# Performance work log

Measured on AMD Instinct MI355X. Metric: run time of the kernel, lower is better.

Reference implementation:

```python
import math
import jax, jax.numpy as jnp
import numpy as np

NEG = -1.0e10  # matches LARGE_NUMBER padding in the original
K_SUBSET = 8
N_SAMPLES = 2


def log_conv(aL, aR, K):
    """Log-space convolution of two count distributions, truncated to counts 0..K-1.
    aL, aR: [..., K] log-values; returns c[m] = logsumexp_j aL[j] + aR[m-j]."""
    jj = jnp.arange(K)[:, None]
    mm = jnp.arange(K)[None, :]
    idx = mm - jj  # [K(j), K(m)]
    valid = idx >= 0
    aRg = aR[..., jnp.clip(idx, 0, K - 1)]  # [..., K, K]
    t = aL[..., :, None] + jnp.where(valid, aRg, NEG)
    return jax.nn.logsumexp(t, axis=-2)


def up_pass(theta, k):
    """theta: [B, N] logits (N power of two). Returns list of per-level log-ESP
    tables, levels[l]: [B, N/2^l, k+1]; levels[-1][:,0,j] = log e_j(exp theta)."""
    B, N = theta.shape
    K = k + 1
    leaf = jnp.full((B, N, K), NEG, theta.dtype)
    leaf = leaf.at[..., 0].set(0.0).at[..., 1].set(theta)
    levels = [leaf]
    a = leaf
    while a.shape[1] > 1:
        a = log_conv(a[:, 0::2], a[:, 1::2], K)
        levels.append(a)
    return levels


def down_marginals(levels, theta, k):
    """Exact inclusion marginals P(x_i=1 | sum=k) via tree forward-backward."""
    K = k + 1
    B = theta.shape[0]
    ext = jnp.full((B, 1, K), NEG, theta.dtype).at[..., 0].set(0.0)
    for lvl in range(len(levels) - 2, -1, -1):
        a = levels[lvl]
        aL, aR = a[:, 0::2], a[:, 1::2]
        extL = log_conv(ext, aR, K)  # ESP of everything outside left subtree
        extR = log_conv(ext, aL, K)
        ext = jnp.stack([extL, extR], axis=2).reshape(B, a.shape[1], K)
    logZ = levels[-1][:, 0, k]  # log e_k over all items
    # P(x_i=1) = exp(theta_i) * e_{k-1}(others) / e_k(all)
    return jnp.exp(theta + ext[..., k - 1] - logZ[:, None])


def sample_counts(levels, k, n_samples, key):
    """Top-down exact sampling of k-subsets; returns leaf counts [S, B, N] in {0,1}."""
    K = k + 1
    B = levels[0].shape[0]
    counts = jnp.full((n_samples, B, 1), k, jnp.int32)
    jj = jnp.arange(K)
    for lvl in range(len(levels) - 2, -1, -1):
        a = levels[lvl]
        aL, aR = a[:, 0::2], a[:, 1::2]
        n = aL.shape[1]
        idx = counts[..., None] - jj  # desired right-count, [S,B,n,K]
        valid = idx >= 0
        aRg = jnp.take_along_axis(
            jnp.broadcast_to(aR[None], (n_samples, B, n, K)),
            jnp.clip(idx, 0, k), axis=-1)
        logits = aL[None] + jnp.where(valid, aRg, NEG)
        key, sub = jax.random.split(key)
        g = jax.random.gumbel(sub, logits.shape, logits.dtype)
        cL = jnp.argmax(logits + g, axis=-1).astype(jnp.int32)
        cR = counts - cL
        counts = jnp.stack([cL, cR], axis=-1).reshape(n_samples, B, 2 * n)
    return counts


def setup_inputs() -> dict:
    key = jax.random.key(0)
    scores = jax.random.normal(key, (8192, 32, 8), dtype=jnp.float32)
    return {"scores": scores}


def reference(scores):
    nnodes, choices, ensemble = scores.shape
    k = min(K_SUBSET, choices)
    flat = jnp.transpose(scores, (0, 2, 1)).reshape(nnodes * ensemble, choices)
    N = 2 ** math.ceil(math.log2(choices))
    if N > choices:
        flat = jnp.concatenate(
            [flat, jnp.full((flat.shape[0], N - choices), NEG, flat.dtype)], axis=1)
    levels = up_pass(flat, k)
    marg_flat = down_marginals(levels, flat, k)[:, :choices]  # [B, choices]
    marginals = jnp.transpose(
        marg_flat.reshape(nnodes, ensemble, choices), (0, 2, 1))  # [nnodes, choices, ensemble]
    counts = sample_counts(levels, k, N_SAMPLES, jax.random.key(42))
    counts = counts[:, :, :choices].astype(scores.dtype)
    samples = jnp.transpose(
        counts.reshape(N_SAMPLES, nnodes, ensemble, choices), (0, 1, 3, 2))
    # straight-through: hard samples forward, marginal gradients backward
    samples = jax.lax.stop_gradient(samples - marginals[None]) + marginals[None]
    return samples, marginals
```

## Files before the change

### kernel.cpp

```cpp
#include <hip/hip_runtime.h>
#include <stdint.h>


__host__ __device__ __forceinline__ void tf2x32(uint32_t k0, uint32_t k1,
                                                uint32_t x0, uint32_t x1,
                                                uint32_t& y0, uint32_t& y1) {
  const uint32_t ks[3] = {k0, k1, k0 ^ k1 ^ 0x1BD11BDAu};
  x0 += ks[0]; x1 += ks[1];
  const int R0[4] = {13, 15, 26, 6};
  const int R1[4] = {17, 29, 16, 24};
#pragma unroll
  for (int i = 0; i < 5; ++i) {
    const int* R = (i & 1) ? R1 : R0;
#pragma unroll
    for (int rr = 0; rr < 4; ++rr) {
      x0 += x1;
      x1 = (x1 << R[rr]) | (x1 >> (32 - R[rr]));
      x1 ^= x0;
    }
    x0 += ks[(i + 1) % 3];
    x1 += ks[(i + 2) % 3] + (uint32_t)(i + 1);
  }
  y0 = x0; y1 = x1;
}

struct TFKeys { uint32_t v[10]; };

__device__ __forceinline__ float gumbel_draw(uint32_t sk0, uint32_t sk1,
                                             uint32_t f) {
  uint32_t y0, y1;
  tf2x32(sk0, sk1, 0u, f, y0, y1);
  uint32_t bits = y0 ^ y1;
  uint32_t fb = (bits >> 9) | 0x3f800000u;
  float u = __uint_as_float(fb) - 1.0f;
  const float tiny = 1.17549435e-38f;
  float rr = fmaxf(tiny, u + tiny);
  return -logf(-logf(rr));
}

template<bool FAST> __device__ __forceinline__ float expT(float x) {
  return FAST ? __expf(x) : expf(x);
}
template<bool FAST> __device__ __forceinline__ float logT(float x) {
  return FAST ? __logf(x) : logf(x);
}

template<int SIN, int SOUT, bool FAST, bool LS>
__device__ __forceinline__ void conv_level(const float (&aL)[SIN],
                                           const float (&aR)[SIN],
                                           float (&o)[SOUT]) {
#pragma unroll
  for (int m = 1; m < SOUT; ++m) {
    if (LS && m == SOUT - 1) { o[m] = aL[SIN - 1] + aR[SIN - 1]; continue; }
    const int jlo = (m - (SIN - 1) > 0) ? (m - (SIN - 1)) : 0;
    const int jhi = (m < SIN - 1) ? m : (SIN - 1);
    float t[SIN];
#pragma unroll
    for (int j = 0; j < SIN; ++j)
      if (j >= jlo && j <= jhi) t[j] = aL[j] + aR[m - j];
    float amax = t[jlo];
#pragma unroll
    for (int j = 0; j < SIN; ++j)
      if (j > jlo && j <= jhi) amax = fmaxf(amax, t[j]);
    float s = 0.0f;
#pragma unroll
    for (int j = 0; j < SIN; ++j)
      if (j >= jlo && j <= jhi) s += expT<FAST>(t[j] - amax);
    o[m] = logT<FAST>(s) + amax;
  }
}

template<int SSIB, int MLO, int MHI, bool FAST>
__device__ __forceinline__ void ext_level(const float (&ein)[8],
                                          const float* sib, float (&eo)[8]) {
#pragma unroll
  for (int m = MLO; m <= MHI; ++m) {
    const int jlo = (m - (SSIB - 1) > 0) ? (m - (SSIB - 1)) : 0;
    float t[8];
#pragma unroll
    for (int j = 0; j < 8; ++j)
      if (j >= jlo && j <= m) t[j] = ein[j] + sib[m - j];
    float amax = t[jlo];
#pragma unroll
    for (int j = 0; j < 8; ++j)
      if (j > jlo && j <= m) amax = fmaxf(amax, t[j]);
    float s = 0.0f;
#pragma unroll
    for (int j = 0; j < 8; ++j)
      if (j >= jlo && j <= m) s += expT<FAST>(t[j] - amax);
    eo[m] = logT<FAST>(s) + amax;
  }
}

#define ENT 128

__global__ __launch_bounds__(64, 2) void simple_sampler_kernel(
    const float* __restrict__ scores, float* __restrict__ out,
    int nnodes, TFKeys keys) {
  const int lane = threadIdx.x;
  const int p = lane & 1;
  const int r = lane >> 1;
  const int row = blockIdx.x * 32 + r;
  const int node = row >> 3, e = row & 7;
  const int B = nnodes * 8;

  __shared__ float tab[ENT * 32];
#define L(E) tab[(E) * 32 + r]

  float th[16];
  const float* sc = scores + node * 256 + e + p * 128;
#pragma unroll
  for (int c = 0; c < 16; ++c) th[c] = sc[c * 8];
#pragma unroll
  for (int c = 0; c < 16; ++c) L(16 * p + c) = th[c];

  float l1r[8], th2r[8];
#pragma unroll
  for (int n1l = 0; n1l < 8; ++n1l) {
    float tL = th[2 * n1l], tR = th[2 * n1l + 1];
    float amax = fmaxf(tR, tL);
    float s = expf(tR - amax) + expf(tL - amax);
    l1r[n1l] = logf(s) + amax;
    th2r[n1l] = tL + tR;
    int n1 = 8 * p + n1l;
    L(32 + n1) = l1r[n1l];
    L(48 + n1) = th2r[n1l];
  }
  float l2r[4][5];
#pragma unroll
  for (int n2l = 0; n2l < 4; ++n2l) {
    float aL[3] = {0.0f, l1r[2 * n2l], th2r[2 * n2l]};
    float aR[3] = {0.0f, l1r[2 * n2l + 1], th2r[2 * n2l + 1]};
    float o5[5];
    conv_level<3, 5, false, true>(aL, aR, o5);
    l2r[n2l][0] = 0.0f;
    int n2 = 4 * p + n2l;
#pragma unroll
    for (int m = 1; m < 5; ++m) { l2r[n2l][m] = o5[m]; L(64 + n2 * 4 + m - 1) = o5[m]; }
  }
  float l3r[2][9];
#pragma unroll
  for (int n3l = 0; n3l < 2; ++n3l) {
    float o9[9];
    conv_level<5, 9, false, true>(l2r[2 * n3l], l2r[2 * n3l + 1], o9);
    l3r[n3l][0] = 0.0f;
    int n3 = 2 * p + n3l;
#pragma unroll
    for (int m = 1; m < 9; ++m) { l3r[n3l][m] = o9[m]; L(96 + n3 * 8 + m - 1) = o9[m]; }
  }

  __builtin_amdgcn_wave_barrier();

  float A0[9], A1[9];
  {
    float l4o[9];
    conv_level<9, 9, false, false>(l3r[0], l3r[1], l4o);
    A0[0] = 0.0f; A1[0] = 0.0f;
#pragma unroll
    for (int m = 1; m < 9; ++m) {
      float own = l4o[m];
      float oth = __shfl_xor(own, 1);
      A0[m] = p ? oth : own;
      A1[m] = p ? own : oth;
    }
  }

  float logZ;
  {
    float tv[9];
#pragma unroll
    for (int j = 0; j < 9; ++j) tv[j] = A0[j] + A1[8 - j];
    float amax = tv[0];
#pragma unroll
    for (int j = 1; j < 9; ++j) amax = fmaxf(amax, tv[j]);
    float s = 0.0f;
#pragma unroll
    for (int j = 0; j < 9; ++j) s += __expf(tv[j] - amax);
    logZ = __logf(s) + amax;
  }

  {
    float e4v[8];
    e4v[0] = 0.0f;
#pragma unroll
    for (int m = 1; m < 8; ++m) e4v[m] = p ? A0[m] : A1[m];
    float* mb = out + 2 * B * 32 + node * 256 + e;
#pragma unroll
    for (int n3l = 0; n3l < 2; ++n3l) {
      float e3[8];
      ext_level<9, 0, 7, true>(e4v, l3r[n3l ^ 1], e3);
#pragma unroll
      for (int c2 = 0; c2 < 2; ++c2) {
        const int n2l = 2 * n3l + c2;
        float e2v[8];
        ext_level<5, 4, 7, true>(e3, l2r[n2l ^ 1], e2v);
#pragma unroll
        for (int c1i = 0; c1i < 2; ++c1i) {
          const int n1l = 2 * n2l + c1i;
          float sib1[3] = {0.0f, l1r[n1l ^ 1], th2r[n1l ^ 1]};
          float e1m[8];
          ext_level<3, 6, 7, true>(e2v, sib1, e1m);
          const int colL = 16 * p + 2 * n1l;
          {
            float t6 = e1m[6] + th[2 * n1l + 1];
            float t7 = e1m[7];
            float amax = fmaxf(t6, t7);
            float s = __expf(t6 - amax) + __expf(t7 - amax);
            mb[colL * 8] = __expf((th[2 * n1l] + (__logf(s) + amax)) - logZ);
          }
          {
            float t6 = e1m[6] + th[2 * n1l];
            float t7 = e1m[7];
            float amax = fmaxf(t6, t7);
            float s = __expf(t6 - amax) + __expf(t7 - amax);
            mb[(colL + 1) * 8] = __expf((th[2 * n1l + 1] + (__logf(s) + amax)) - logZ);
          }
        }
      }
    }
  }

  const uint32_t t9 = (uint32_t)(p * B + row) * 9u;
  int c0, c1;
  {
    float best = 0.0f; int bj = 0;
#pragma unroll
    for (int j = 0; j < 9; ++j) {
      float g = gumbel_draw(keys.v[0], keys.v[1], t9 + (uint32_t)j);
      float v = (A0[j] + A1[8 - j]) + g;
      if (j == 0) { best = v; } else if (v > best) { best = v; bj = j; }
    }
    c0 = bj; c1 = 8 - bj;
  }
  int c1v[4];
  {
    const int n0 = c0 ? c0 + 1 : 0;
    const int n1c = c1 ? c1 + 1 : 0;
    const int tot = n0 + n1c;
    float b0 = -3.0e38f, b1 = -3.0e38f;
    int j0 = 0, j1 = 0;
    for (int t = 0; t < tot; ++t) {
      const bool is1 = (t >= n0);
      const int j = is1 ? (t - n0) : t;
      const int c = is1 ? c1 : c0;
      const int i = is1 ? 1 : 0;
      const int idx = c - j;
      float a = (j == 0) ? 0.0f : L(96 + 16 * i + j - 1);
      float b = (idx == 0) ? 0.0f : L(96 + 16 * i + 8 + idx - 1);
      float g = gumbel_draw(keys.v[2], keys.v[3],
                            2u * t9 + (uint32_t)(9 * i + j));
      float v = (a + b) + g;
      if (is1) { if (v > b1) { b1 = v; j1 = j; } }
      else     { if (v > b0) { b0 = v; j0 = j; } }
    }
    c1v[0] = j0; c1v[1] = c0 - j0; c1v[2] = j1; c1v[3] = c1 - j1;
  }
  uint32_t pk2 = 0;
  {
#pragma unroll
    for (int i = 0; i < 4; ++i) {
      int c = c1v[i];
      float best = -3.0e38f; int bj2 = 0;
#pragma unroll
      for (int j = 0; j < 5; ++j) {
        float g = gumbel_draw(keys.v[4], keys.v[5],
                              4u * t9 + (uint32_t)(i * 9 + j));
        int idx = c - j;
        int cl = min(max(idx, 1), 4);
        float b = L(64 + (2 * i + 1) * 4 + cl - 1);
        float bf = (idx == 0) ? 0.0f : b;
        float a = (j == 0) ? 0.0f : L(64 + (2 * i) * 4 + j - 1);
        float v = (a + bf) + g;
        if (idx >= 0 && idx <= 4 && v > best) { best = v; bj2 = j; }
      }
      pk2 |= ((uint32_t)bj2 << (8 * i)) | ((uint32_t)(c - bj2) << (8 * i + 4));
    }
  }
  uint64_t pk64 = 0;
  {
    const uint32_t sk0 = keys.v[6], sk1 = keys.v[7];
    const uint32_t fb0 = 8u * t9;
#pragma unroll 2
    for (int i = 0; i < 8; ++i) {
      int c = (int)((pk2 >> (4 * i)) & 15u);
      float aL1 = L(32 + 2 * i), aL2 = L(48 + 2 * i);
      float bR1 = L(32 + 2 * i + 1), bR2 = L(48 + 2 * i + 1);
      uint32_t fb = fb0 + (uint32_t)(i * 9);
      float best = -3.0e38f; int bj3 = 0;
#pragma unroll
      for (int j = 0; j < 3; ++j) {
        float g = gumbel_draw(sk0, sk1, fb + (uint32_t)j);
        int idx = c - j;
        float bf = (idx == 1) ? bR1 : ((idx == 2) ? bR2 : 0.0f);
        float af = (j == 0) ? 0.0f : ((j == 1) ? aL1 : aL2);
        float v = (af + bf) + g;
        if (idx >= 0 && idx <= 2 && v > best) { best = v; bj3 = j; }
      }
      pk64 |= ((uint64_t)(uint32_t)bj3 << (8 * i)) |
              ((uint64_t)(uint32_t)(c - bj3) << (8 * i + 4));
    }
  }
  {
    const uint32_t sk0 = keys.v[8], sk1 = keys.v[9];
    const uint32_t fb0 = 16u * t9;
    float* bs = out + p * (B * 32) + node * 256 + e;
    uint64_t lst = 0; int m4 = 0;
#pragma unroll
    for (int i = 0; i < 16; ++i) {
      int c = (int)((uint32_t)(pk64 >> (4 * i)) & 15u);
      if (c == 1) {
        lst |= ((uint64_t)(uint32_t)i) << (4 * m4);
        ++m4;
      } else {
        int bj = c >> 1;
        bs[16 * i] = (float)bj;
        bs[16 * i + 8] = (float)(c - bj);
      }
    }
    for (int tt = 0; tt < m4; ++tt) {
      int i = (int)((lst >> (4 * tt)) & 15u);
      float thL = L(2 * i);
      float thR = L(2 * i + 1);
      uint32_t fb = fb0 + (uint32_t)(i * 9);
      float g0 = gumbel_draw(sk0, sk1, fb);
      float g1 = gumbel_draw(sk0, sk1, fb + 1u);
      int bj = ((thL + g1) > (thR + g0)) ? 1 : 0;
      bs[16 * i] = (float)bj;
      bs[16 * i + 8] = (float)(1 - bj);
    }
  }
#undef L
}

extern "C" void kernel_launch(void* const* d_in, const int* in_sizes, int n_in,
                              void* d_out, int out_size, void* d_ws, size_t ws_size,
                              hipStream_t stream) {
  const float* scores = (const float*)d_in[0];
  float* out = (float*)d_out;
  const int nnodes = in_sizes[0] / (32 * 8);
  const int B = nnodes * 8;

  TFKeys K;
  uint32_t k0 = 0u, k1 = 42u;
  for (int t = 0; t < 5; ++t) {
    uint32_t n0, n1, s0, s1;
    tf2x32(k0, k1, 0u, 0u, n0, n1);
    tf2x32(k0, k1, 0u, 1u, s0, s1);
    K.v[2 * t] = s0; K.v[2 * t + 1] = s1;
    k0 = n0; k1 = n1;
  }

  dim3 grid((unsigned)(B / 32)), block(64);
  hipLaunchKernelGGL(simple_sampler_kernel, grid, block, 0, stream,
                     scores, out, nnodes, K);
}
```

Before: 114.4 us.

## Split each row across four lanes instead of two and enlarge blocks

Each row (node, ensemble) is now handled by four lanes rather than two. Each lane holds 8 logits and does a quarter of the up-pass tree, exchanging level-3 tables with a shuffle. Sampling is split across lanes by sample index and by left/right half of the tree, with the root choice combined through a shuffle. Blocks grow from one wave to four waves with per-wave shared tables, which raises parallelism and cuts per-thread registers, at the cost of extra shuffles and some redundant root work.

Measured after the change: 115.2 us. About the same (+0.6%).

```diff
diff --git a/kernel.cpp b/kernel.cpp
--- a/kernel.cpp
+++ b/kernel.cpp
@@ -94,67 +94,81 @@
 
 #define ENT 128
 
-__global__ __launch_bounds__(64, 2) void simple_sampler_kernel(
+__global__ __launch_bounds__(256, 4) void simple_sampler_kernel(
     const float* __restrict__ scores, float* __restrict__ out,
     int nnodes, TFKeys keys) {
-  const int lane = threadIdx.x;
-  const int p = lane & 1;
-  const int r = lane >> 1;
-  const int row = blockIdx.x * 32 + r;
+  const int wl = threadIdx.x & 63;
+  const int w  = threadIdx.x >> 6;
+  const int q = wl & 3;
+  const int r = wl >> 2;
+  const int p = q & 1;
+  const int g = q >> 1;
+  const int row = blockIdx.x * 64 + w * 16 + r;
   const int node = row >> 3, e = row & 7;
   const int B = nnodes * 8;
 
-  __shared__ float tab[ENT * 32];
-#define L(E) tab[(E) * 32 + r]
-
-  float th[16];
-  const float* sc = scores + node * 256 + e + p * 128;
-#pragma unroll
-  for (int c = 0; c < 16; ++c) th[c] = sc[c * 8];
-#pragma unroll
-  for (int c = 0; c < 16; ++c) L(16 * p + c) = th[c];
-
-  float l1r[8], th2r[8];
-#pragma unroll
-  for (int n1l = 0; n1l < 8; ++n1l) {
+  __shared__ float tab[4 * ENT * 16];
+  float* tw = tab + w * (ENT * 16);
+#define L(E) tw[(E) * 16 + r]
+
+  float th[8];
+  const float* sc = scores + node * 256 + e + (16 * p + 8 * g) * 8;
+#pragma unroll
+  for (int c = 0; c < 8; ++c) th[c] = sc[c * 8];
+#pragma unroll
+  for (int c = 0; c < 8; ++c) L(16 * p + 8 * g + c) = th[c];
+
+  float l1r[4], th2r[4];
+#pragma unroll
+  for (int n1l = 0; n1l < 4; ++n1l) {
     float tL = th[2 * n1l], tR = th[2 * n1l + 1];
     float amax = fmaxf(tR, tL);
     float s = expf(tR - amax) + expf(tL - amax);
     l1r[n1l] = logf(s) + amax;
     th2r[n1l] = tL + tR;
-    int n1 = 8 * p + n1l;
+    int n1 = 8 * p + 4 * g + n1l;
     L(32 + n1) = l1r[n1l];
     L(48 + n1) = th2r[n1l];
   }
-  float l2r[4][5];
-#pragma unroll
-  for (int n2l = 0; n2l < 4; ++n2l) {
+  float l2r[2][5];
+#pragma unroll
+  for (int n2l = 0; n2l < 2; ++n2l) {
     float aL[3] = {0.0f, l1r[2 * n2l], th2r[2 * n2l]};
     float aR[3] = {0.0f, l1r[2 * n2l + 1], th2r[2 * n2l + 1]};
     float o5[5];
     conv_level<3, 5, false, true>(aL, aR, o5);
     l2r[n2l][0] = 0.0f;
-    int n2 = 4 * p + n2l;
+    int n2 = 4 * p + 2 * g + n2l;
 #pragma unroll
     for (int m = 1; m < 5; ++m) { l2r[n2l][m] = o5[m]; L(64 + n2 * 4 + m - 1) = o5[m]; }
   }
-  float l3r[2][9];
-#pragma unroll
-  for (int n3l = 0; n3l < 2; ++n3l) {
+  float l3r[9];
+  {
     float o9[9];
-    conv_level<5, 9, false, true>(l2r[2 * n3l], l2r[2 * n3l + 1], o9);
-    l3r[n3l][0] = 0.0f;
-    int n3 = 2 * p + n3l;
-#pragma unroll
-    for (int m = 1; m < 9; ++m) { l3r[n3l][m] = o9[m]; L(96 + n3 * 8 + m - 1) = o9[m]; }
+    conv_level<5, 9, false, true>(l2r[0], l2r[1], o9);
+    l3r[0] = 0.0f;
+    int n3 = 2 * p + g;
+#pragma unroll
+    for (int m = 1; m < 9; ++m) { l3r[m] = o9[m]; L(96 + n3 * 8 + m - 1) = o9[m]; }
   }
 
   __builtin_amdgcn_wave_barrier();
 
+  float l3s[9];
+  l3s[0] = 0.0f;
+#pragma unroll
+  for (int m = 1; m < 9; ++m) l3s[m] = __shfl_xor(l3r[m], 2);
+
   float A0[9], A1[9];
   {
+    float aLp[9], aRp[9];
+#pragma unroll
+    for (int m = 0; m < 9; ++m) {
+      aLp[m] = g ? l3s[m] : l3r[m];
+      aRp[m] = g ? l3r[m] : l3s[m];
+    }
     float l4o[9];
-    conv_level<9, 9, false, false>(l3r[0], l3r[1], l4o);
+    conv_level<9, 9, false, false>(aLp, aRp, l4o);
     A0[0] = 0.0f; A1[0] = 0.0f;
 #pragma unroll
     for (int m = 1; m < 9; ++m) {
@@ -185,140 +199,141 @@
 #pragma unroll
     for (int m = 1; m < 8; ++m) e4v[m] = p ? A0[m] : A1[m];
     float* mb = out + 2 * B * 32 + node * 256 + e;
-#pragma unroll
-    for (int n3l = 0; n3l < 2; ++n3l) {
-      float e3[8];
-      ext_level<9, 0, 7, true>(e4v, l3r[n3l ^ 1], e3);
-#pragma unroll
-      for (int c2 = 0; c2 < 2; ++c2) {
-        const int n2l = 2 * n3l + c2;
-        float e2v[8];
-        ext_level<5, 4, 7, true>(e3, l2r[n2l ^ 1], e2v);
-#pragma unroll
-        for (int c1i = 0; c1i < 2; ++c1i) {
-          const int n1l = 2 * n2l + c1i;
-          float sib1[3] = {0.0f, l1r[n1l ^ 1], th2r[n1l ^ 1]};
-          float e1m[8];
-          ext_level<3, 6, 7, true>(e2v, sib1, e1m);
-          const int colL = 16 * p + 2 * n1l;
-          {
-            float t6 = e1m[6] + th[2 * n1l + 1];
-            float t7 = e1m[7];
-            float amax = fmaxf(t6, t7);
-            float s = __expf(t6 - amax) + __expf(t7 - amax);
-            mb[colL * 8] = __expf((th[2 * n1l] + (__logf(s) + amax)) - logZ);
-          }
-          {
-            float t6 = e1m[6] + th[2 * n1l];
-            float t7 = e1m[7];
-            float amax = fmaxf(t6, t7);
-            float s = __expf(t6 - amax) + __expf(t7 - amax);
-            mb[(colL + 1) * 8] = __expf((th[2 * n1l + 1] + (__logf(s) + amax)) - logZ);
-          }
+    float e3[8];
+    ext_level<9, 0, 7, true>(e4v, l3s, e3);
+#pragma unroll
+    for (int c2 = 0; c2 < 2; ++c2) {
+      float e2v[8];
+      ext_level<5, 4, 7, true>(e3, l2r[c2 ^ 1], e2v);
+#pragma unroll
+      for (int c1i = 0; c1i < 2; ++c1i) {
+        const int n1l = 2 * c2 + c1i;
+        float sib1[3] = {0.0f, l1r[n1l ^ 1], th2r[n1l ^ 1]};
+        float e1m[8];
+        ext_level<3, 6, 7, true>(e2v, sib1, e1m);
+        const int colL = 16 * p + 8 * g + 2 * n1l;
+        {
+          float t6 = e1m[6] + th[2 * n1l + 1];
+          float t7 = e1m[7];
+          float amax = fmaxf(t6, t7);
+          float s = __expf(t6 - amax) + __expf(t7 - amax);
+          mb[colL * 8] = __expf((th[2 * n1l] + (__logf(s) + amax)) - logZ);
         }
-      }
-    }
-  }
-
-  const uint32_t t9 = (uint32_t)(p * B + row) * 9u;
-  int c0, c1;
-  {
-    float best = 0.0f; int bj = 0;
-#pragma unroll
-    for (int j = 0; j < 9; ++j) {
-      float g = gumbel_draw(keys.v[0], keys.v[1], t9 + (uint32_t)j);
-      float v = (A0[j] + A1[8 - j]) + g;
-      if (j == 0) { best = v; } else if (v > best) { best = v; bj = j; }
-    }
-    c0 = bj; c1 = 8 - bj;
-  }
-  int c1v[4];
-  {
-    const int n0 = c0 ? c0 + 1 : 0;
-    const int n1c = c1 ? c1 + 1 : 0;
-    const int tot = n0 + n1c;
-    float b0 = -3.0e38f, b1 = -3.0e38f;
-    int j0 = 0, j1 = 0;
-    for (int t = 0; t < tot; ++t) {
-      const bool is1 = (t >= n0);
-      const int j = is1 ? (t - n0) : t;
-      const int c = is1 ? c1 : c0;
-      const int i = is1 ? 1 : 0;
-      const int idx = c - j;
-      float a = (j == 0) ? 0.0f : L(96 + 16 * i + j - 1);
-      float b = (idx == 0) ? 0.0f : L(96 + 16 * i + 8 + idx - 1);
-      float g = gumbel_draw(keys.v[2], keys.v[3],
-                            2u * t9 + (uint32_t)(9 * i + j));
-      float v = (a + b) + g;
-      if (is1) { if (v > b1) { b1 = v; j1 = j; } }
-      else     { if (v > b0) { b0 = v; j0 = j; } }
-    }
-    c1v[0] = j0; c1v[1] = c0 - j0; c1v[2] = j1; c1v[3] = c1 - j1;
+        {
+          float t6 = e1m[6] + th[2 * n1l];
+          float t7 = e1m[7];
+          float amax = fmaxf(t6, t7);
+          float s = __expf(t6 - amax) + __expf(t7 - amax);
+          mb[(colL + 1) * 8] = __expf((th[2 * n1l + 1] + (__logf(s) + amax)) - logZ);
+        }
+      }
+    }
+  }
+
+  const int smp = q & 1;
+  const int h = q >> 1;
+  const uint32_t t9 = (uint32_t)(smp * B + row) * 9u;
+  int c;
+  {
+    float bv = 0.0f; int bj = 0;
+#pragma unroll
+    for (int k = 0; k < 5; ++k) {
+      const int j = 4 * h + k;
+      float gd = gumbel_draw(keys.v[0], keys.v[1], t9 + (uint32_t)j);
+      float v = (A0[j] + A1[8 - j]) + gd;
+      if (k == 0) { bv = v; bj = j; } else if (v > bv) { bv = v; bj = j; }
+    }
+    float ov = __shfl_xor(bv, 2);
+    int   oj = __shfl_xor(bj, 2);
+    float vlo = h ? ov : bv;  int jlo = h ? oj : bj;
+    float vhi = h ? bv : ov;  int jhi = h ? bj : oj;
+    int rootj = (vhi > vlo) ? jhi : jlo;
+    c = h ? (8 - rootj) : rootj;
+  }
+  int cA, cB;
+  {
+    int j0 = 0;
+    if (c > 0) {
+      float b0 = -3.0e38f;
+      for (int j = 0; j <= c; ++j) {
+        float a = (j == 0) ? 0.0f : L(96 + 16 * h + j - 1);
+        float b = (c - j == 0) ? 0.0f : L(96 + 16 * h + 8 + (c - j) - 1);
+        float gd = gumbel_draw(keys.v[2], keys.v[3],
+                               2u * t9 + (uint32_t)(9 * h + j));
+        float v = (a + b) + gd;
+        if (v > b0) { b0 = v; j0 = j; }
+      }
+    }
+    cA = j0; cB = c - j0;
   }
   uint32_t pk2 = 0;
   {
-#pragma unroll
-    for (int i = 0; i < 4; ++i) {
-      int c = c1v[i];
+    int cc0 = cA, cc1 = cB;
+#pragma unroll
+    for (int i2 = 0; i2 < 2; ++i2) {
+      const int i = 2 * h + i2;
+      int ci = i2 ? cc1 : cc0;
       float best = -3.0e38f; int bj2 = 0;
 #pragma unroll
       for (int j = 0; j < 5; ++j) {
-        float g = gumbel_draw(keys.v[4], keys.v[5],
-                              4u * t9 + (uint32_t)(i * 9 + j));
-        int idx = c - j;
+        float gd = gumbel_draw(keys.v[4], keys.v[5],
+                               4u * t9 + (uint32_t)(i * 9 + j));
+        int idx = ci - j;
         int cl = min(max(idx, 1), 4);
         float b = L(64 + (2 * i + 1) * 4 + cl - 1);
         float bf = (idx == 0) ? 0.0f : b;
         float a = (j == 0) ? 0.0f : L(64 + (2 * i) * 4 + j - 1);
-        float v = (a + bf) + g;
+        float v = (a + bf) + gd;
         if (idx >= 0 && idx <= 4 && v > best) { best = v; bj2 = j; }
       }
-      pk2 |= ((uint32_t)bj2 << (8 * i)) | ((uint32_t)(c - bj2) << (8 * i + 4));
-    }
-  }
-  uint64_t pk64 = 0;
+      pk2 |= ((uint32_t)bj2 << (8 * i2)) | ((uint32_t)(ci - bj2) << (8 * i2 + 4));
+    }
+  }
+  uint32_t pk3 = 0;
   {
     const uint32_t sk0 = keys.v[6], sk1 = keys.v[7];
     const uint32_t fb0 = 8u * t9;
-#pragma unroll 2
-    for (int i = 0; i < 8; ++i) {
-      int c = (int)((pk2 >> (4 * i)) & 15u);
+#pragma unroll
+    for (int i2 = 0; i2 < 4; ++i2) {
+      const int i = 4 * h + i2;
+      int ci = (int)((pk2 >> (4 * i2)) & 15u);
       float aL1 = L(32 + 2 * i), aL2 = L(48 + 2 * i);
       float bR1 = L(32 + 2 * i + 1), bR2 = L(48 + 2 * i + 1);
       uint32_t fb = fb0 + (uint32_t)(i * 9);
       float best = -3.0e38f; int bj3 = 0;
 #pragma unroll
       for (int j = 0; j < 3; ++j) {
-        float g = gumbel_draw(sk0, sk1, fb + (uint32_t)j);
-        int idx = c - j;
+        float gd = gumbel_draw(sk0, sk1, fb + (uint32_t)j);
+        int idx = ci - j;
         float bf = (idx == 1) ? bR1 : ((idx == 2) ? bR2 : 0.0f);
         float af = (j == 0) ? 0.0f : ((j == 1) ? aL1 : aL2);
-        float v = (af + bf) + g;
+        float v = (af + bf) + gd;
         if (idx >= 0 && idx <= 2 && v > best) { best = v; bj3 = j; }
       }
-      pk64 |= ((uint64_t)(uint32_t)bj3 << (8 * i)) |
-              ((uint64_t)(uint32_t)(c - bj3) << (8 * i + 4));
+      pk3 |= ((uint32_t)bj3 << (8 * i2)) | ((uint32_t)(ci - bj3) << (8 * i2 + 4));
     }
   }
   {
     const uint32_t sk0 = keys.v[8], sk1 = keys.v[9];
     const uint32_t fb0 = 16u * t9;
-    float* bs = out + p * (B * 32) + node * 256 + e;
-    uint64_t lst = 0; int m4 = 0;
-#pragma unroll
-    for (int i = 0; i < 16; ++i) {
-      int c = (int)((uint32_t)(pk64 >> (4 * i)) & 15u);
-      if (c == 1) {
-        lst |= ((uint64_t)(uint32_t)i) << (4 * m4);
+    float* bs = out + smp * (B * 32) + node * 256 + e;
+    uint32_t lst = 0; int m4 = 0;
+#pragma unroll
+    for (int i2 = 0; i2 < 8; ++i2) {
+      int ci = (int)((pk3 >> (4 * i2)) & 15u);
+      const int i = 8 * h + i2;
+      if (ci == 1) {
+        lst |= ((uint32_t)i2) << (4 * m4);
         ++m4;
       } else {
-        int bj = c >> 1;
+        int bj = ci >> 1;
         bs[16 * i] = (float)bj;
-        bs[16 * i + 8] = (float)(c - bj);
+        bs[16 * i + 8] = (float)(ci - bj);
       }
     }
     for (int tt = 0; tt < m4; ++tt) {
-      int i = (int)((lst >> (4 * tt)) & 15u);
+      int i2 = (int)((lst >> (4 * tt)) & 15u);
+      int i = 8 * h + i2;
       float thL = L(2 * i);
       float thR = L(2 * i + 1);
       uint32_t fb = fb0 + (uint32_t)(i * 9);
@@ -350,7 +365,7 @@
     k0 = n0; k1 = n1;
   }
 
-  dim3 grid((unsigned)(B / 32)), block(64);
+  dim3 grid((unsigned)(B / 64)), block(256);
   hipLaunchKernelGGL(simple_sampler_kernel, grid, block, 0, stream,
                      scores, out, nnodes, K);
 }
```
